# Kernel tuning notes

Measured on AMD Instinct MI355X. Metric: run time of the kernel, lower is better.

Reference implementation:

```python
import jax, jax.numpy as jnp
import numpy as np

MAX_DISP = 48
B, C, H, W = 2, 32, 128, 240


def setup_inputs() -> dict:
    key = jax.random.key(0)
    k1, k2 = jax.random.split(key)
    l_fmap = jax.random.normal(k1, (B, C, H, W), dtype=jnp.float32)
    r_fmap = jax.random.normal(k2, (B, C, H, W), dtype=jnp.float32)
    return {"l_fmap": l_fmap, "r_fmap": r_fmap}


def reference(l_fmap, r_fmap):
    # Output: [B, C, D, H, W] where out[..., d, :, w] =
    #   l[..., w] - r[..., w-d]  if w >= d else 1.0 (pad value)
    D = MAX_DISP
    Wdim = l_fmap.shape[-1]
    w = jnp.arange(Wdim)                       # [W]
    d = jnp.arange(D)[:, None]                 # [D,1]
    shift_idx = jnp.maximum(w[None, :] - d, 0) # [D,W], clamped gather index
    # Gather shifted right features: [B,C,H,W] indexed on last axis by [D,W] -> [B,C,H,D,W]
    r_shifted = r_fmap[..., shift_idx]
    r_shifted = jnp.transpose(r_shifted, (0, 1, 3, 2, 4))  # [B,C,D,H,W]
    diff = l_fmap[:, :, None, :, :] - r_shifted            # [B,C,D,H,W]
    valid = (w[None, :] >= d)                              # [D,W]
    cost_volume = jnp.where(valid[None, None, :, None, :], diff,
                            jnp.float32(1.0))
    return cost_volume
```

## Files before the change

kernel.cpp:

```cpp
#include <hip/hip_runtime.h>


#define MAX_DISP 48
#define HH 128
#define WW 240
#define NV 60
#define PAD4 12

typedef float f32x4 __attribute__((ext_vector_type(4)));

__global__ __launch_bounds__(256) void costvol_kernel(
    const f32x4* __restrict__ l4,
    const float* __restrict__ r,
    f32x4* __restrict__ out4)
{
    __shared__ float r_pad[48 + WW];

    const int bch = blockIdx.x;
    const int h   = bch % HH;
    const int bc  = bch / HH;
    const int tid = threadIdx.x;
    const int v   = tid & 63;
    const int kg  = tid >> 6;

    if (tid < 48)  r_pad[tid] = 0.0f;
    if (tid < WW)  r_pad[48 + tid] = r[(size_t)bch * WW + tid];

    f32x4 lv = {0.f, 0.f, 0.f, 0.f};
    if (v < NV) lv = l4[(size_t)bch * NV + v];
    __syncthreads();

    if (v >= NV) return;

    const f32x4* rp4 = (const f32x4*)r_pad;
    const size_t  dstride4 = (size_t)HH * NV;
    const int     w0 = 4 * v;

    #pragma unroll
    for (int iter = 0; iter < 3; ++iter) {
        const int k  = kg + 4 * iter;
        const int d0 = 4 * k;

        f32x4 A = rp4[PAD4 + v - k];
        f32x4 B = rp4[PAD4 + v - k - 1];

        size_t ob = ((size_t)(bc * MAX_DISP + d0) * HH + h) * NV + v;

        #pragma unroll
        for (int s = 0; s < 4; ++s) {
            f32x4 o;
            #pragma unroll
            for (int j = 0; j < 4; ++j) {
                const int src = j - s;
                float rv = (src >= 0) ? A[src] : B[4 + src];
                o[j] = (w0 + j >= d0 + s) ? (lv[j] - rv) : 1.0f;
            }
            __builtin_nontemporal_store(o, &out4[ob + (size_t)s * dstride4]);
        }
    }
}

extern "C" void kernel_launch(void* const* d_in, const int* in_sizes, int n_in,
                              void* d_out, int out_size, void* d_ws, size_t ws_size,
                              hipStream_t stream) {
    const f32x4* l4 = (const f32x4*)d_in[0];
    const float* r  = (const float*)d_in[1];
    f32x4* out4 = (f32x4*)d_out;

    const int nblocks = 2 * 32 * HH;
    costvol_kernel<<<nblocks, 256, 0, stream>>>(l4, r, out4);
}
```

Baseline: 77.59 us.

## Process 16 rows per block with one thread per float4, all disparities

Restructures the work split so each 960-thread block handles 16 rows of one (b,c) slice. Each thread owns one float4 column and loops over all 48 disparities instead of 12. Rows are loaded into LDS as float4 with zero padding, and the threads left idle by the old 64-wide layout are removed. This cuts the block count and per-block setup cost, but puts more stores on each thread and makes blocks large, which may limit occupancy or how stores interleave. Output is 94 MB of writes, so the kernel is bandwidth-bound.

```diff
diff --git a/kernel.cpp b/kernel.cpp
--- a/kernel.cpp
+++ b/kernel.cpp
@@ -6,45 +6,42 @@
 #define WW 240
 #define NV 60
 #define PAD4 12
+#define ROW4 (PAD4 + NV)
+#define HG 16
 
 typedef float f32x4 __attribute__((ext_vector_type(4)));
 
-__global__ __launch_bounds__(256) void costvol_kernel(
+__global__ __launch_bounds__(960) void costvol_kernel(
     const f32x4* __restrict__ l4,
-    const float* __restrict__ r,
+    const f32x4* __restrict__ r4,
     f32x4* __restrict__ out4)
 {
-    __shared__ float r_pad[48 + WW];
+    __shared__ f32x4 r_lds[HG * ROW4];
 
-    const int bch = blockIdx.x;
-    const int h   = bch % HH;
-    const int bc  = bch / HH;
+    const int bc  = blockIdx.x & 63;
+    const int hg  = blockIdx.x >> 6;
+    const int h0  = hg * HG;
     const int tid = threadIdx.x;
-    const int v   = tid & 63;
-    const int kg  = tid >> 6;
+    const int hl  = tid / NV;
+    const int v   = tid % NV;
 
-    if (tid < 48)  r_pad[tid] = 0.0f;
-    if (tid < WW)  r_pad[48 + tid] = r[(size_t)bch * WW + tid];
-
-    f32x4 lv = {0.f, 0.f, 0.f, 0.f};
-    if (v < NV) lv = l4[(size_t)bch * NV + v];
+    if (tid < HG * PAD4) {
+        r_lds[(tid / PAD4) * ROW4 + (tid % PAD4)] = (f32x4){0.f, 0.f, 0.f, 0.f};
+    }
+    const size_t in_base = ((size_t)bc * HH + h0) * NV;
+    r_lds[hl * ROW4 + PAD4 + v] = r4[in_base + tid];
+    const f32x4 lv = l4[in_base + tid];
     __syncthreads();
 
-    if (v >= NV) return;
-
-    const f32x4* rp4 = (const f32x4*)r_pad;
-    const size_t  dstride4 = (size_t)HH * NV;
-    const int     w0 = 4 * v;
+    const int w0 = 4 * v;
+    size_t ob = ((size_t)bc * MAX_DISP * HH + h0 + hl) * NV + v;
+    const size_t dstride4 = (size_t)HH * NV;
 
     #pragma unroll
-    for (int iter = 0; iter < 3; ++iter) {
-        const int k  = kg + 4 * iter;
+    for (int k = 0; k < MAX_DISP / 4; ++k) {
         const int d0 = 4 * k;
-
-        f32x4 A = rp4[PAD4 + v - k];
-        f32x4 B = rp4[PAD4 + v - k - 1];
-
-        size_t ob = ((size_t)(bc * MAX_DISP + d0) * HH + h) * NV + v;
+        const f32x4 A = r_lds[hl * ROW4 + PAD4 + v - k];
+        const f32x4 B = r_lds[hl * ROW4 + PAD4 + v - k - 1];
 
         #pragma unroll
         for (int s = 0; s < 4; ++s) {
@@ -55,7 +52,7 @@
                 float rv = (src >= 0) ? A[src] : B[4 + src];
                 o[j] = (w0 + j >= d0 + s) ? (lv[j] - rv) : 1.0f;
             }
-            __builtin_nontemporal_store(o, &out4[ob + (size_t)s * dstride4]);
+            __builtin_nontemporal_store(o, &out4[ob + (size_t)(d0 + s) * dstride4]);
         }
     }
 }
@@ -64,9 +61,9 @@
                               void* d_out, int out_size, void* d_ws, size_t ws_size,
                               hipStream_t stream) {
     const f32x4* l4 = (const f32x4*)d_in[0];
-    const float* r  = (const float*)d_in[1];
+    const f32x4* r4 = (const f32x4*)d_in[1];
     f32x4* out4 = (f32x4*)d_out;
 
-    const int nblocks = 2 * 32 * HH;
-    costvol_kernel<<<nblocks, 256, 0, stream>>>(l4, r, out4);
+    const int nblocks = 64 * (HH / HG);
+    costvol_kernel<<<nblocks, 960, 0, stream>>>(l4, r4, out4);
 }
```

Result: slower. 79.56 us (+2.5%).
